# Optimization experiments

Measured on AMD Instinct MI355X. Metric: run time of the kernel, lower is better.

## Reference

```python
import jax, jax.numpy as jnp
import numpy as np

B, T, D = 4, 2048, 1024
H = 16
HD = D // H  # 64


def setup_inputs() -> dict:
    key = jax.random.key(0)
    k1, k2, k3 = jax.random.split(key, 3)
    x = jax.random.normal(k1, (B, T, D), dtype=jnp.float32)
    w_qkv = jax.random.normal(k2, (D, 3 * D), dtype=jnp.float32) * (1.0 / np.sqrt(D))
    w_out = jax.random.normal(k3, (D, D), dtype=jnp.float32) * (1.0 / np.sqrt(D))
    return {"x": x, "w_qkv": w_qkv, "w_out": w_out}


def reference(x, w_qkv, w_out):
    b, t, c = x.shape
    qkv = x @ w_qkv  # [B,T,3D]
    q, k, v = jnp.split(qkv, 3, axis=-1)

    def heads(u):
        return u.reshape(b, t, H, HD).transpose(0, 2, 1, 3)  # [B,H,T,HD]

    q, k, v = heads(q), heads(k), heads(v)
    scale = 1.0 / np.sqrt(HD).astype(np.float32)
    attn = jnp.einsum('bhqd,bhkd->bhqk', q, k) * scale  # [B,H,T,T]
    causal = jnp.tril(jnp.ones((t, t), dtype=bool))
    attn = jnp.where(causal[None, None, :, :], attn, -jnp.inf)
    attn = jax.nn.softmax(attn, axis=-1)
    y = jnp.einsum('bhqk,bhkd->bhqd', attn, v)  # [B,H,T,HD]
    y = y.transpose(0, 2, 1, 3).reshape(b, t, c)
    return y @ w_out
```

## Files before the change

kernel.cpp:

```cpp
#include <hip/hip_runtime.h>
#include <hip/hip_bf16.h>
#include <stdint.h>

#define B_    4
#define T_    2048
#define D_    1024
#define H_    16
#define HD_   64
#define ROWS_ (B_ * T_)
#define NQKV_ (3 * D_)

typedef __attribute__((ext_vector_type(8))) short bf16x8;
typedef __attribute__((ext_vector_type(4))) float f32x4;

__device__ __forceinline__ unsigned short f2bf(float f) {
    union { float f; uint32_t u; } v; v.f = f;
    uint32_t u = v.u;
    return (unsigned short)((u + 0x7FFFu + ((u >> 16) & 1u)) >> 16);
}

__device__ __forceinline__ uint32_t pack2_rtz(float a, float b) {
    union { float f; uint32_t u; } x, y; x.f = a; y.f = b;
    return (x.u >> 16) | (y.u & 0xFFFF0000u);
}

__device__ __forceinline__ void glds16(const unsigned short* g, unsigned short* l) {
    __builtin_amdgcn_global_load_lds(
        (const __attribute__((address_space(1))) void*)g,
        (__attribute__((address_space(3))) void*)l, 16, 0, 0);
}

__global__ void cvt_bf16_kernel(const float* __restrict__ in,
                                unsigned short* __restrict__ out, int n8) {
    int i = blockIdx.x * blockDim.x + threadIdx.x;
    if (i >= n8) return;
    float4 a = ((const float4*)in)[2 * i];
    float4 b = ((const float4*)in)[2 * i + 1];
    union { bf16x8 v; unsigned short s[8]; } o;
    o.s[0] = f2bf(a.x); o.s[1] = f2bf(a.y); o.s[2] = f2bf(a.z); o.s[3] = f2bf(a.w);
    o.s[4] = f2bf(b.x); o.s[5] = f2bf(b.y); o.s[6] = f2bf(b.z); o.s[7] = f2bf(b.w);
    ((bf16x8*)out)[i] = o.v;
}

__global__ __launch_bounds__(256) void tcvt_kernel(const float* __restrict__ in,
                                                   unsigned short* __restrict__ out,
                                                   int K, int N, int ncut, float scale) {
    __shared__ float tile[64 * 65];
    const int t = threadIdx.x;
    const int n0 = blockIdx.x * 64, k0 = blockIdx.y * 64;
#pragma unroll
    for (int it = 0; it < 4; ++it) {
        int id = it * 256 + t;
        int r = id >> 4, c = (id & 15) * 4;
        float4 v = *(const float4*)&in[(size_t)(k0 + r) * N + n0 + c];
        tile[r * 65 + c + 0] = v.x; tile[r * 65 + c + 1] = v.y;
        tile[r * 65 + c + 2] = v.z; tile[r * 65 + c + 3] = v.w;
    }
    __syncthreads();
#pragma unroll
    for (int it = 0; it < 2; ++it) {
        int id = it * 256 + t;
        int n = id >> 3, kc = (id & 7) * 8;
        float sc = (n0 + n < ncut) ? scale : 1.0f;
        union { bf16x8 v; unsigned short s[8]; } o;
#pragma unroll
        for (int i = 0; i < 8; ++i) o.s[i] = f2bf(tile[(kc + i) * 65 + n] * sc);
        *(bf16x8*)&out[(size_t)(n0 + n) * K + k0 + kc] = o.v;
    }
}

template<int OUT_BF16, int VSPLIT>
__global__ __launch_bounds__(256) void gemm128_kernel(
    const unsigned short* __restrict__ A,
    const unsigned short* __restrict__ Bt,
    void* __restrict__ Cp, int M, int K, int ldC,
    unsigned short* __restrict__ vt)
{
    __shared__ __align__(16) unsigned short As[128 * 32];
    __shared__ __align__(16) unsigned short Bs[128 * 32];

    const int t = threadIdx.x, w = t >> 6, lane = t & 63;
    const int wm = w >> 1, wn = w & 1;
    const int lm = lane & 15, lq = lane >> 4;
    const int m0 = blockIdx.y * 128, n0 = blockIdx.x * 128;

    f32x4 acc[4][4];
#pragma unroll
    for (int i = 0; i < 4; i++)
#pragma unroll
        for (int j = 0; j < 4; j++) acc[i][j] = (f32x4){0.f, 0.f, 0.f, 0.f};

    const int id0 = t, id1 = 256 + t;
    const unsigned short* Ap0 = A + (size_t)(m0 + (id0 >> 2)) * K + (id0 & 3) * 8;
    const unsigned short* Ap1 = A + (size_t)(m0 + (id1 >> 2)) * K + (id1 & 3) * 8;
    const unsigned short* Bp0 = Bt + (size_t)(n0 + (id0 >> 2)) * K + (id0 & 3) * 8;
    const unsigned short* Bp1 = Bt + (size_t)(n0 + (id1 >> 2)) * K + (id1 & 3) * 8;

    for (int k0 = 0; k0 < K; k0 += 32) {
        __syncthreads();
        glds16(Ap0 + k0, &As[id0 * 8]);
        glds16(Ap1 + k0, &As[id1 * 8]);
        glds16(Bp0 + k0, &Bs[id0 * 8]);
        glds16(Bp1 + k0, &Bs[id1 * 8]);
        __syncthreads();

        bf16x8 af[4], bfr[4];
#pragma unroll
        for (int mt = 0; mt < 4; mt++)
            af[mt] = *(const bf16x8*)&As[(wm * 64 + mt * 16 + lm) * 32 + lq * 8];
#pragma unroll
        for (int nt = 0; nt < 4; nt++)
            bfr[nt] = *(const bf16x8*)&Bs[(wn * 64 + nt * 16 + lm) * 32 + lq * 8];
#pragma unroll
        for (int mt = 0; mt < 4; mt++)
#pragma unroll
            for (int nt = 0; nt < 4; nt++)
                acc[mt][nt] = __builtin_amdgcn_mfma_f32_16x16x32_bf16(
                    af[mt], bfr[nt], acc[mt][nt], 0, 0, 0);
    }

    if (VSPLIT && n0 >= 2048) {
#pragma unroll
        for (int mt = 0; mt < 4; mt++)
#pragma unroll
            for (int nt = 0; nt < 4; nt++) {
                int row0 = m0 + wm * 64 + mt * 16 + lq * 4;
                int col  = n0 + wn * 64 + nt * 16 + lm - 2048;
                int bb = row0 >> 11, tt = row0 & 2047;
                size_t vi = ((size_t)((bb * 16 + (col >> 6)) * 64 + (col & 63))) * 2048 + tt;
                uint2 pk;
                pk.x = (uint32_t)f2bf(acc[mt][nt][0]) | ((uint32_t)f2bf(acc[mt][nt][1]) << 16);
                pk.y = (uint32_t)f2bf(acc[mt][nt][2]) | ((uint32_t)f2bf(acc[mt][nt][3]) << 16);
                *(uint2*)&vt[vi] = pk;
            }
        return;
    }
#pragma unroll
    for (int mt = 0; mt < 4; mt++)
#pragma unroll
        for (int nt = 0; nt < 4; nt++)
#pragma unroll
            for (int r = 0; r < 4; r++) {
                int row = m0 + wm * 64 + mt * 16 + lq * 4 + r;
                int col = n0 + wn * 64 + nt * 16 + lm;
                if (OUT_BF16)
                    ((unsigned short*)Cp)[(size_t)row * ldC + col] = f2bf(acc[mt][nt][r]);
                else
                    ((float*)Cp)[(size_t)row * ldC + col] = acc[mt][nt][r];
            }
}

__global__ __launch_bounds__(256) void attn4_kernel(
    const unsigned short* __restrict__ qk,
    const unsigned short* __restrict__ vt,
    unsigned short* __restrict__ y)
{
    __shared__ __align__(16) unsigned short Ks[64 * 72];
    __shared__ __align__(16) unsigned short Vs[64 * 72];
    __shared__ __align__(16) unsigned short Ps[4][32 * 72];

    const int bh = blockIdx.x, pair = blockIdx.y;
    const int b = bh >> 4, h = bh & 15;
    const int t = threadIdx.x, w = t >> 6, lane = t & 63;
    const int lm = lane & 15, lq = lane >> 4;
    unsigned short* psw = Ps[w];

    const int r0 = t >> 3,           c0 = (t & 7) * 8;
    const int r1 = (256 + t) >> 3,   c1 = (t & 7) * 8;
    const unsigned short* kgb = qk + (size_t)(b * T_) * 2048 + D_ + h * HD_;
    const unsigned short* vgb = vt + (size_t)(bh * 64) * 2048;

    const bf16x8 onesf = {0x3F80, 0x3F80, 0x3F80, 0x3F80,
                          0x3F80, 0x3F80, 0x3F80, 0x3F80};

    for (int which = 0; which < 2; ++which) {
        const int qt = which ? pair : (15 - pair);
        const int q0 = qt * 128, qw0 = q0 + w * 32;

        bf16x8 qf[2][2];
#pragma unroll
        for (int mt = 0; mt < 2; mt++)
#pragma unroll
            for (int kk = 0; kk < 2; kk++)
                qf[mt][kk] = *(const bf16x8*)
                    &qk[(size_t)(b * T_ + qw0 + mt * 16 + lm) * 2048 + h * HD_ + kk * 32 + lq * 8];

        f32x4 o[2][4], osum[2];
#pragma unroll
        for (int mt = 0; mt < 2; mt++) {
            osum[mt] = (f32x4){0.f, 0.f, 0.f, 0.f};
#pragma unroll
            for (int dt = 0; dt < 4; dt++) o[mt][dt] = (f32x4){0.f, 0.f, 0.f, 0.f};
        }

        const int kend = q0 + 128;

        bf16x8 ka = *(const bf16x8*)&kgb[(size_t)(0 + r0) * 2048 + c0];
        bf16x8 kb = *(const bf16x8*)&kgb[(size_t)(0 + r1) * 2048 + c1];
        bf16x8 va = *(const bf16x8*)&vgb[(size_t)r0 * 2048 + 0 + c0];
        bf16x8 vb = *(const bf16x8*)&vgb[(size_t)r1 * 2048 + 0 + c1];

        for (int kt = 0; kt < kend; kt += 64) {
            __syncthreads();
            *(bf16x8*)&Ks[r0 * 72 + c0] = ka;
            *(bf16x8*)&Ks[r1 * 72 + c1] = kb;
            *(bf16x8*)&Vs[r0 * 72 + c0] = va;
            *(bf16x8*)&Vs[r1 * 72 + c1] = vb;
            int ktn = (kt + 64 < kend) ? kt + 64 : kt;
            ka = *(const bf16x8*)&kgb[(size_t)(ktn + r0) * 2048 + c0];
            kb = *(const bf16x8*)&kgb[(size_t)(ktn + r1) * 2048 + c1];
            va = *(const bf16x8*)&vgb[(size_t)r0 * 2048 + ktn + c0];
            vb = *(const bf16x8*)&vgb[(size_t)r1 * 2048 + ktn + c1];
            __syncthreads();
            if (kt >= qw0 + 32) continue;

            f32x4 st[4][2];
#pragma unroll
            for (int nt = 0; nt < 4; nt++)
#pragma unroll
                for (int mt = 0; mt < 2; mt++) st[nt][mt] = (f32x4){0.f, 0.f, 0.f, 0.f};
#pragma unroll
            for (int nt = 0; nt < 4; nt++)
#pragma unroll
                for (int kk = 0; kk < 2; kk++) {
                    bf16x8 kf = *(const bf16x8*)&Ks[(nt * 16 + lm) * 72 + kk * 32 + lq * 8];
#pragma unroll
                    for (int mt = 0; mt < 2; mt++)
                        st[nt][mt] = __builtin_amdgcn_mfma_f32_16x16x32_bf16(
                            kf, qf[mt][kk], st[nt][mt], 0, 0, 0);
                }

            const bool diag = (kt + 64 > qw0);
#pragma unroll
            for (int mt = 0; mt < 2; mt++) {
                const int qi = qw0 + mt * 16 + lm;
#pragma unroll
                for (int nt = 0; nt < 4; nt++) {
                    float p[4];
                    if (diag) {
                        const int kj0 = kt + nt * 16 + lq * 4;
#pragma unroll
                        for (int r = 0; r < 4; r++)
                            p[r] = (kj0 + r <= qi)
                                 ? __builtin_amdgcn_exp2f(st[nt][mt][r]) : 0.f;
                    } else {
#pragma unroll
                        for (int r = 0; r < 4; r++)
                            p[r] = __builtin_amdgcn_exp2f(st[nt][mt][r]);
                    }
                    uint2 pk;
                    pk.x = pack2_rtz(p[0], p[1]);
                    pk.y = pack2_rtz(p[2], p[3]);
                    *(uint2*)&psw[(mt * 16 + lm) * 72 + nt * 16 + lq * 4] = pk;
                }
            }

#pragma unroll
            for (int kk = 0; kk < 2; kk++) {
                bf16x8 pf0 = *(const bf16x8*)&psw[(lm) * 72 + kk * 32 + lq * 8];
                bf16x8 pf1 = *(const bf16x8*)&psw[(16 + lm) * 72 + kk * 32 + lq * 8];
                osum[0] = __builtin_amdgcn_mfma_f32_16x16x32_bf16(pf0, onesf, osum[0], 0, 0, 0);
                osum[1] = __builtin_amdgcn_mfma_f32_16x16x32_bf16(pf1, onesf, osum[1], 0, 0, 0);
#pragma unroll
                for (int dt = 0; dt < 4; dt++) {
                    bf16x8 vf = *(const bf16x8*)&Vs[(dt * 16 + lm) * 72 + kk * 32 + lq * 8];
                    o[0][dt] = __builtin_amdgcn_mfma_f32_16x16x32_bf16(pf0, vf, o[0][dt], 0, 0, 0);
                    o[1][dt] = __builtin_amdgcn_mfma_f32_16x16x32_bf16(pf1, vf, o[1][dt], 0, 0, 0);
                }
            }
        }

#pragma unroll
        for (int mt = 0; mt < 2; mt++)
#pragma unroll
            for (int r = 0; r < 4; r++) {
                float rli = 1.f / osum[mt][r];
#pragma unroll
                for (int dt = 0; dt < 4; dt++)
                    y[(size_t)(b * T_ + qw0 + mt * 16 + lq * 4 + r) * D_ + h * HD_ + dt * 16 + lm]
                        = f2bf(o[mt][dt][r] * rli);
            }
    }
}

extern "C" void kernel_launch(void* const* d_in, const int* in_sizes, int n_in,
                              void* d_out, int out_size, void* d_ws, size_t ws_size,
                              hipStream_t stream) {
    const float* x    = (const float*)d_in[0];
    const float* wqkv = (const float*)d_in[1];
    const float* wout = (const float*)d_in[2];
    float* out = (float*)d_out;

    char* ws = (char*)d_ws;
    unsigned short* xb     = (unsigned short*)ws; ws += (size_t)ROWS_ * D_ * 2;
    unsigned short* wqkvbt = (unsigned short*)ws; ws += (size_t)D_ * NQKV_ * 2;
    unsigned short* woutbt = (unsigned short*)ws; ws += (size_t)D_ * D_ * 2;
    unsigned short* qkb    = (unsigned short*)ws; ws += (size_t)ROWS_ * 2048 * 2;
    unsigned short* vtb    = (unsigned short*)ws; ws += (size_t)ROWS_ * D_ * 2;
    unsigned short* yb     = (unsigned short*)ws;

    const float SC = 0.18033688011112042f;

    cvt_bf16_kernel<<<ROWS_ * D_ / 8 / 256, 256, 0, stream>>>(x, xb, ROWS_ * D_ / 8);
    tcvt_kernel<<<dim3(NQKV_ / 64, D_ / 64), 256, 0, stream>>>(wqkv, wqkvbt, D_, NQKV_, D_, SC);
    tcvt_kernel<<<dim3(D_ / 64, D_ / 64), 256, 0, stream>>>(wout, woutbt, D_, D_, 0, 1.0f);

    gemm128_kernel<1, 1><<<dim3(NQKV_ / 128, ROWS_ / 128), 256, 0, stream>>>(
        xb, wqkvbt, qkb, ROWS_, D_, 2048, vtb);

    attn4_kernel<<<dim3(B_ * H_, 8), 256, 0, stream>>>(qkb, vtb, yb);

    gemm128_kernel<0, 0><<<dim3(D_ / 128, ROWS_ / 128), 256, 0, stream>>>(
        yb, woutbt, out, ROWS_, D_, D_, nullptr);
}
```

Measured before the change: 260.6 us.

## Double GEMM K-tile to 64 with XOR-swizzled LDS and merge weight transposes

The GEMM kernel now stages a 64-wide K slice per iteration instead of 32. This halves the number of barrier pairs and doubles the MFMA work between syncs. LDS chunks are XOR-swizzled by row to avoid bank conflicts on the wider rows. The two weight transpose-convert launches are also merged into one kernel to save a launch. The cost is doubled LDS per block, which may reduce occupancy.

```diff
diff --git a/kernel.cpp b/kernel.cpp
--- a/kernel.cpp
+++ b/kernel.cpp
@@ -42,12 +42,21 @@
     ((bf16x8*)out)[i] = o.v;
 }
 
-__global__ __launch_bounds__(256) void tcvt_kernel(const float* __restrict__ in,
-                                                   unsigned short* __restrict__ out,
-                                                   int K, int N, int ncut, float scale) {
+__global__ __launch_bounds__(256) void tcvt2_kernel(const float* __restrict__ wqkv,
+                                                    const float* __restrict__ wout,
+                                                    unsigned short* __restrict__ oqkv,
+                                                    unsigned short* __restrict__ oout,
+                                                    float scale) {
     __shared__ float tile[64 * 65];
     const int t = threadIdx.x;
-    const int n0 = blockIdx.x * 64, k0 = blockIdx.y * 64;
+    const bool second = blockIdx.x >= 48;
+    const float* in = second ? wout : wqkv;
+    unsigned short* out = second ? oout : oqkv;
+    const int N = second ? 1024 : 3072;
+    const int ncut = second ? 0 : 1024;
+    const int n0 = (second ? (blockIdx.x - 48) : blockIdx.x) * 64;
+    const int k0 = blockIdx.y * 64;
+    const int K = 1024;
 #pragma unroll
     for (int it = 0; it < 4; ++it) {
         int id = it * 256 + t;
@@ -76,8 +85,8 @@
     void* __restrict__ Cp, int M, int K, int ldC,
     unsigned short* __restrict__ vt)
 {
-    __shared__ __align__(16) unsigned short As[128 * 32];
-    __shared__ __align__(16) unsigned short Bs[128 * 32];
+    __shared__ __align__(16) unsigned short As[128 * 64];
+    __shared__ __align__(16) unsigned short Bs[128 * 64];
 
     const int t = threadIdx.x, w = t >> 6, lane = t & 63;
     const int wm = w >> 1, wn = w & 1;
@@ -90,33 +99,46 @@
 #pragma unroll
         for (int j = 0; j < 4; j++) acc[i][j] = (f32x4){0.f, 0.f, 0.f, 0.f};
 
-    const int id0 = t, id1 = 256 + t;
-    const unsigned short* Ap0 = A + (size_t)(m0 + (id0 >> 2)) * K + (id0 & 3) * 8;
-    const unsigned short* Ap1 = A + (size_t)(m0 + (id1 >> 2)) * K + (id1 & 3) * 8;
-    const unsigned short* Bp0 = Bt + (size_t)(n0 + (id0 >> 2)) * K + (id0 & 3) * 8;
-    const unsigned short* Bp1 = Bt + (size_t)(n0 + (id1 >> 2)) * K + (id1 & 3) * 8;
-
-    for (int k0 = 0; k0 < K; k0 += 32) {
+    const unsigned short* Ap[4];
+    const unsigned short* Bp[4];
+#pragma unroll
+    for (int s = 0; s < 4; s++) {
+        int id = s * 256 + t;
+        int row = id >> 3, gch = (id & 7) ^ (row & 7);
+        Ap[s] = A  + (size_t)(m0 + row) * K + gch * 8;
+        Bp[s] = Bt + (size_t)(n0 + row) * K + gch * 8;
+    }
+
+    for (int k0 = 0; k0 < K; k0 += 64) {
         __syncthreads();
-        glds16(Ap0 + k0, &As[id0 * 8]);
-        glds16(Ap1 + k0, &As[id1 * 8]);
-        glds16(Bp0 + k0, &Bs[id0 * 8]);
-        glds16(Bp1 + k0, &Bs[id1 * 8]);
+#pragma unroll
+        for (int s = 0; s < 4; s++) glds16(Ap[s] + k0, &As[(s * 256 + t) * 8]);
+#pragma unroll
+        for (int s = 0; s < 4; s++) glds16(Bp[s] + k0, &Bs[(s * 256 + t) * 8]);
         __syncthreads();
 
-        bf16x8 af[4], bfr[4];
-#pragma unroll
-        for (int mt = 0; mt < 4; mt++)
-            af[mt] = *(const bf16x8*)&As[(wm * 64 + mt * 16 + lm) * 32 + lq * 8];
-#pragma unroll
-        for (int nt = 0; nt < 4; nt++)
-            bfr[nt] = *(const bf16x8*)&Bs[(wn * 64 + nt * 16 + lm) * 32 + lq * 8];
-#pragma unroll
-        for (int mt = 0; mt < 4; mt++)
-#pragma unroll
-            for (int nt = 0; nt < 4; nt++)
-                acc[mt][nt] = __builtin_amdgcn_mfma_f32_16x16x32_bf16(
-                    af[mt], bfr[nt], acc[mt][nt], 0, 0, 0);
+#pragma unroll
+        for (int kh = 0; kh < 2; kh++) {
+            bf16x8 af[4], bfr[4];
+#pragma unroll
+            for (int mt = 0; mt < 4; mt++) {
+                int row = wm * 64 + mt * 16 + lm;
+                int sch = (kh * 4 + lq) ^ (lm & 7);
+                af[mt] = *(const bf16x8*)&As[row * 64 + sch * 8];
+            }
+#pragma unroll
+            for (int nt = 0; nt < 4; nt++) {
+                int row = wn * 64 + nt * 16 + lm;
+                int sch = (kh * 4 + lq) ^ (lm & 7);
+                bfr[nt] = *(const bf16x8*)&Bs[row * 64 + sch * 8];
+            }
+#pragma unroll
+            for (int mt = 0; mt < 4; mt++)
+#pragma unroll
+                for (int nt = 0; nt < 4; nt++)
+                    acc[mt][nt] = __builtin_amdgcn_mfma_f32_16x16x32_bf16(
+                        af[mt], bfr[nt], acc[mt][nt], 0, 0, 0);
+        }
     }
 
     if (VSPLIT && n0 >= 2048) {
@@ -302,8 +324,7 @@
     const float SC = 0.18033688011112042f;
 
     cvt_bf16_kernel<<<ROWS_ * D_ / 8 / 256, 256, 0, stream>>>(x, xb, ROWS_ * D_ / 8);
-    tcvt_kernel<<<dim3(NQKV_ / 64, D_ / 64), 256, 0, stream>>>(wqkv, wqkvbt, D_, NQKV_, D_, SC);
-    tcvt_kernel<<<dim3(D_ / 64, D_ / 64), 256, 0, stream>>>(wout, woutbt, D_, D_, 0, 1.0f);
+    tcvt2_kernel<<<dim3(64, 16), 256, 0, stream>>>(wqkv, wout, wqkvbt, woutbt, SC);
 
     gemm128_kernel<1, 1><<<dim3(NQKV_ / 128, ROWS_ / 128), 256, 0, stream>>>(
         xb, wqkvbt, qkb, ROWS_, D_, 2048, vtb);
```

After: 242.0 us. -7.2%, faster.
